# Kernel tuning notes

Hardware: AMD Instinct MI355X
Metric: run time of the kernel (lower is better)

The kernel has to match this reference:

```python
import jax, jax.numpy as jnp
import numpy as np

B, N, HID, NH, NREL, E = 4, 1024, 768, 12, 64, 65536
DH = HID // NH  # 64
TOKEN_TYPE = 0  # NodeType.TOKEN.value


def setup_inputs() -> dict:
    key = jax.random.key(0)
    ks = jax.random.split(key, 24)
    s = 0.02
    inp = {}
    inp["node_states"] = jax.random.normal(ks[0], (B, N, HID), jnp.float32)
    eb = jax.random.randint(ks[1], (E,), 0, B)
    eh = jax.random.randint(ks[2], (E,), 0, N)
    et = jax.random.randint(ks[3], (E,), 0, N)
    er = jax.random.randint(ks[4], (E,), 0, NREL)
    inp["edge_indices"] = jnp.stack([eb, eh, et, er]).astype(jnp.int32)
    inp["node_type_ids"] = jax.random.randint(ks[5], (B, N), 0, 3).astype(jnp.int32)
    names = ["Wq", "Wk", "Wv", "Wq_kb", "Wk_kb", "Wv_kb"]
    for i, nm in enumerate(names):
        inp[nm] = jax.random.normal(ks[6 + i], (HID, HID), jnp.float32) * s
        inp["b" + nm[1:]] = jax.random.normal(ks[12 + i], (HID,), jnp.float32) * s
    inp["rel_mats"] = jax.random.normal(ks[18], (NREL, DH, DH), jnp.float32) * s
    edge_emb = jax.random.normal(ks[19], (NREL, HID), jnp.float32) * s
    inp["edge_emb"] = edge_emb.at[0].set(0.0)  # TOKEN_TO_TOKEN_RELATION_ID row zeroed
    return inp


def reference(node_states, edge_indices, node_type_ids,
              Wq, bq, Wk, bk, Wv, bv,
              Wq_kb, bq_kb, Wk_kb, bk_kb, Wv_kb, bv_kb,
              rel_mats, edge_emb):
    eb, eh, et, er = edge_indices  # (E,) each
    tok = (node_type_ids == TOKEN_TYPE)[..., None]  # (B, N, 1)

    def dual(W_tok, b_tok, W_kb, b_kb):
        # mask_a * tok_proj(x) + mask_b * kb_proj(x)
        return jnp.where(tok, node_states @ W_tok.T + b_tok,
                         node_states @ W_kb.T + b_kb)

    Q = dual(Wq, bq, Wq_kb, bq_kb)  # (B, N, HID)
    K = dual(Wk, bk, Wk_kb, bk_kb)
    V = dual(Wv, bv, Wv_kb, bv_kb)

    # --- attention logits on edges ---
    Qe = Q[eb, eh].reshape(E, NH, DH)  # query at head node
    Ke = K[eb, et].reshape(E, NH, DH)  # key at tail node
    Me = rel_mats[er]                  # (E, DH, DH) per-edge relation matrix
    # (Q @ M) . K per head, scaled
    logits = jnp.einsum('ehd,edf,ehf->eh', Qe, Me, Ke) / jnp.sqrt(
        jnp.asarray(DH, node_states.dtype))  # (E, NH)

    # --- sparse softmax over tail nodes, per (batch, head_node, att_head) ---
    seg = eb * N + eh  # (E,)
    mx = jax.ops.segment_max(logits, seg, num_segments=B * N)  # (B*N, NH)
    ex = jnp.exp(logits - mx[seg])
    denom = jax.ops.segment_sum(ex, seg, num_segments=B * N)
    probs = ex / denom[seg]  # (E, NH); dropout p=0.0 (eval)

    # --- values: V at tail node + edge value embedding ---
    Ve = (V[eb, et] + edge_emb[er]).reshape(E, NH, DH)

    # --- weighted scatter-sum over tail dim ---
    msg = probs[..., None] * Ve  # (E, NH, DH)
    out = jax.ops.segment_sum(msg, seg, num_segments=B * N)  # (B*N, NH, DH)
    return out.reshape(B, N, HID)
```

## Files before the change

### kernel.cpp

```cpp
#include <hip/hip_runtime.h>
#include <math.h>
#include <stdint.h>

#define BB   4
#define NN   1024
#define HID  768
#define NH   12
#define DH   64
#define NREL 64
#define EE   65536
#define NSEG (BB*NN)
#define NOUT 4608
#define UNIT_E 64
#define MAXU (EE/UNIT_E + NREL)
#define NBLK 256
#define MAXMT 34

typedef __bf16 bf16;
typedef __bf16 bf16x8 __attribute__((ext_vector_type(8)));
typedef float  f32x4  __attribute__((ext_vector_type(4)));

__device__ __forceinline__ void load_lds16(const void* g, void* l) {
  __builtin_amdgcn_global_load_lds(
      (__attribute__((address_space(1))) void*)(uintptr_t)g,
      (__attribute__((address_space(3))) void*)(uintptr_t)l, 16, 0, 0);
}

__device__ __forceinline__ int swz(int byte_off) {
  return byte_off ^ (((byte_off >> 7) & 7) << 4);
}

__device__ __forceinline__ float b2f(unsigned short u) {
  return __uint_as_float(((unsigned)u) << 16);
}

__global__ __launch_bounds__(1024)
void partition_kernel(const int* __restrict__ nt, int* __restrict__ origrow,
                      int* __restrict__ meta, int* __restrict__ cnt){
  __shared__ int sums[1024];
  __shared__ int ntot;
  const int t = threadIdx.x;
  int tk[4]; int c = 0;
  #pragma unroll
  for (int i=0;i<4;i++){ tk[i] = (nt[t*4+i]==0); c += tk[i]; cnt[t*4+i] = 0; }
  sums[t]=c; __syncthreads();
  for (int off=1; off<1024; off<<=1){
    const int v = (t>=off) ? sums[t-off] : 0;
    __syncthreads();
    sums[t]+=v;
    __syncthreads();
  }
  if (t==1023) ntot = sums[1023];
  __syncthreads();
  const int excl = sums[t]-c;
  int tokpos = excl, kbpos = ntot + (4*t - excl);
  #pragma unroll
  for (int i=0;i<4;i++){
    if (tk[i]) origrow[tokpos++] = t*4+i;
    else       origrow[kbpos++]  = t*4+i;
  }
  if (t==0){
    const int ntok = ntot, nkb = NSEG - ntok;
    const int tt = (ntok+127)>>7, ktt = (nkb+127)>>7;
    meta[0]=ntok; meta[1]=tt+ktt;
    for (int m=0;m<tt+ktt;m++){
      meta[2+m]  = (m<tt) ? m*128 : ntok + (m-tt)*128;
      meta[40+m] = (m<tt) ? 1 : 0;
    }
  }
}

__global__ __launch_bounds__(256)
void prep_kernel(const float* __restrict__ X, const int* __restrict__ origrow,
                 const float* __restrict__ W0, const float* __restrict__ W1,
                 const float* __restrict__ W2, const float* __restrict__ W3,
                 const float* __restrict__ W4, const float* __restrict__ W5,
                 const float* __restrict__ b0, const float* __restrict__ b1,
                 const float* __restrict__ b2, const float* __restrict__ b3,
                 const float* __restrict__ b4, const float* __restrict__ b5,
                 const float* __restrict__ relm, const float* __restrict__ emb,
                 bf16* __restrict__ Xp, bf16* __restrict__ Wb,
                 float* __restrict__ biasAll, bf16* __restrict__ Mt,
                 bf16* __restrict__ Eb){
  const int blk = blockIdx.x, tid = threadIdx.x;
  if (blk < NSEG) {
    if (tid < 192) {
      const int orig = origrow[blk];
      float4 v = *reinterpret_cast<const float4*>(X + (size_t)orig*HID + tid*4);
      bf16 o[4] = {(bf16)v.x,(bf16)v.y,(bf16)v.z,(bf16)v.w};
      *reinterpret_cast<uint64_t*>(Xp + (size_t)blk*HID + tid*4) = *reinterpret_cast<uint64_t*>(o);
    }
  } else if (blk < NSEG + NOUT) {
    const int r = blk - NSEG;
    const int j = r / HID;
    const int o = r - j * HID;
    const float* Wj; const float* bj;
    if      (j==0){Wj=W0;bj=b0;} else if(j==1){Wj=W1;bj=b1;}
    else if (j==2){Wj=W2;bj=b2;} else if(j==3){Wj=W3;bj=b3;}
    else if (j==4){Wj=W4;bj=b4;} else            {Wj=W5;bj=b5;}
    const float* src = Wj + (size_t)o * HID;
    bf16* dst = Wb + (size_t)r * HID;
    for (int c = tid; c < HID; c += 256) dst[c] = (bf16)src[c];
    if (tid == 0) biasAll[r] = bj[o];
  } else if (blk < NSEG + NOUT + NREL) {
    const int r = blk - NSEG - NOUT;
    const float* M = relm + (size_t)r * DH * DH;
    bf16* o = Mt + (size_t)r * DH * DH;
    for (int i = tid; i < DH * DH; i += 256) {
      const int d = i >> 6, f = i & 63;
      o[f * DH + d] = (bf16)M[i];
    }
  } else {
    const int r = blk - NSEG - NOUT - NREL;
    const float* src = emb + (size_t)r * HID;
    bf16* dst = Eb + (size_t)r * HID;
    for (int c = tid; c < HID; c += 256) dst[c] = (bf16)src[c];
  }
}

#define BM 128
#define BN 128
#define BK 32
#define NT (HID/BK)
#define NCT 18
#define NWG (MAXMT*NCT)

__global__ __launch_bounds__(256)
void gemm_kernel(const bf16* __restrict__ A, const bf16* __restrict__ Bw,
                 const float* __restrict__ biasAll, const int* __restrict__ origrow,
                 const int* __restrict__ meta,
                 bf16* __restrict__ Qb, bf16* __restrict__ Kb, bf16* __restrict__ Vb)
{
  __shared__ bf16 As[3][BM * BK];
  __shared__ bf16 Bs[3][BN * BK];

  const int orig = blockIdx.x;
  const int xcd  = orig & 7;
  const int wg   = (xcd < 4 ? xcd * 77 : 4 * 77 + (xcd - 4) * 76) + (orig >> 3);
  const int mt   = wg / NCT;
  const int ctt  = wg - mt * NCT;

  const int ntok = meta[0], nmt = meta[1];
  if (mt >= nmt) return;
  const int base  = meta[2+mt];
  const int istok = meta[40+mt];

  const int tid  = threadIdx.x;
  const int lane = tid & 63;
  const int w    = tid >> 6;
  const int wrow = w >> 1, wcol = w & 1;
  const int ct_local = ctt * BN;
  const int brow0 = (istok ? 0 : 2304) + ct_local;

  f32x4 acc[4][4];
  #pragma unroll
  for (int mi=0;mi<4;mi++)
    #pragma unroll
    for (int ni=0;ni<4;ni++) acc[mi][ni] = (f32x4){0.f,0.f,0.f,0.f};

  const char* Ab = (const char*)A;
  const char* Bb = (const char*)Bw;

  int rowg[2], inrowg[2], Pg[2];
  #pragma unroll
  for (int i = 0; i < 2; ++i) {
    const int P = (i * 256 + tid) * 16;
    const int L = swz(P);
    Pg[i] = P; rowg[i] = L >> 6; inrowg[i] = L & 63;
  }

  #define STAGE(kt, b)                                                              \
    { _Pragma("unroll")                                                             \
      for (int i = 0; i < 2; ++i) {                                                 \
        load_lds16(Ab + ((size_t)(base  + rowg[i]) * HID + (kt) * BK) * 2 + inrowg[i], \
                   (char*)As[b] + Pg[i]);                                           \
        load_lds16(Bb + ((size_t)(brow0 + rowg[i]) * HID + (kt) * BK) * 2 + inrowg[i], \
                   (char*)Bs[b] + Pg[i]);                                           \
      } }

  STAGE(0, 0);
  STAGE(1, 1);

  for (int kt = 0; kt < NT; ++kt) {
    if (kt < NT - 1) asm volatile("s_waitcnt vmcnt(4)" ::: "memory");
    else             asm volatile("s_waitcnt vmcnt(0)" ::: "memory");
    __builtin_amdgcn_s_barrier();
    if (kt + 2 < NT) { STAGE(kt + 2, (kt + 2) % 3); }

    const char* Asb = (const char*)As[kt % 3];
    const char* Bsb = (const char*)Bs[kt % 3];
    bf16x8 af[4], bfr[4];
    #pragma unroll
    for (int mi = 0; mi < 4; ++mi) {
      const int r = wrow * 64 + mi * 16 + (lane & 15);
      const int L = r * 64 + (lane >> 4) * 16;
      af[mi] = *reinterpret_cast<const bf16x8*>(Asb + swz(L));
    }
    #pragma unroll
    for (int ni = 0; ni < 4; ++ni) {
      const int r = wcol * 64 + ni * 16 + (lane & 15);
      const int L = r * 64 + (lane >> 4) * 16;
      bfr[ni] = *reinterpret_cast<const bf16x8*>(Bsb + swz(L));
    }
    #pragma unroll
    for (int mi = 0; mi < 4; ++mi)
      #pragma unroll
      for (int ni = 0; ni < 4; ++ni)
        acc[mi][ni] = __builtin_amdgcn_mfma_f32_16x16x32_bf16(af[mi], bfr[ni], acc[mi][ni], 0, 0, 0);
  }

  const int j3 = ct_local / HID;
  const int o0 = ct_local - j3 * HID;
  const int rowLim = istok ? ntok : NSEG;
  const int bidx0 = (istok ? j3 : j3 + 3) * HID + o0;
  #pragma unroll
  for (int mi = 0; mi < 4; ++mi) {
    #pragma unroll
    for (int i = 0; i < 4; ++i) {
      const int rr = base + wrow * 64 + mi * 16 + (lane >> 4) * 4 + i;
      if (rr < rowLim) {
        const int orig2 = origrow[rr];
        #pragma unroll
        for (int ni = 0; ni < 4; ++ni) {
          const int cg = wcol * 64 + ni * 16 + (lane & 15);
          const float val = acc[mi][ni][i] + biasAll[bidx0 + cg];
          if (j3 == 2)      Vb[(size_t)orig2 * HID + o0 + cg] = (bf16)val;
          else if (j3 == 0) Qb[(size_t)orig2 * HID + o0 + cg] = (bf16)val;
          else              Kb[(size_t)orig2 * HID + o0 + cg] = (bf16)val;
        }
      }
    }
  }
}

__global__ __launch_bounds__(256)
void hist_both_kernel(const int* __restrict__ ei, int* __restrict__ cnt,
                      int* __restrict__ cnt_blk){
  __shared__ int lc[NREL];
  const int tid = threadIdx.x, blk = blockIdx.x;
  if (tid < NREL) lc[tid] = 0;
  __syncthreads();
  const int e = blk*256 + tid;
  atomicAdd(&cnt[ei[e]*NN + ei[EE+e]], 1);
  atomicAdd(&lc[ei[3*EE+e]], 1);
  __syncthreads();
  if (tid < NREL) cnt_blk[tid*NBLK + blk] = lc[tid];
}

__global__ __launch_bounds__(1024)
void scan_both_kernel(const int* __restrict__ cnt, int* __restrict__ start,
                      int* __restrict__ cursor, int* __restrict__ cnt_blk,
                      int* __restrict__ start_rel, int* __restrict__ cnt_rel,
                      int* __restrict__ ustart){
  __shared__ int sums[1024];
  const int t = threadIdx.x;
  if (blockIdx.x == 0) {
    const int c0=cnt[t*4], c1=cnt[t*4+1], c2=cnt[t*4+2], c3=cnt[t*4+3];
    const int s = c0+c1+c2+c3;
    sums[t]=s; __syncthreads();
    for (int off=1; off<1024; off<<=1){
      const int v = (t>=off) ? sums[t-off] : 0;
      __syncthreads();
      sums[t]+=v;
      __syncthreads();
    }
    const int excl = sums[t]-s;
    const int o0=excl, o1=o0+c0, o2=o1+c1, o3=o2+c2;
    start[t*4]=o0;  start[t*4+1]=o1;  start[t*4+2]=o2;  start[t*4+3]=o3;
    cursor[t*4]=o0; cursor[t*4+1]=o1; cursor[t*4+2]=o2; cursor[t*4+3]=o3;
  } else {
    int v[16]; int s = 0;
    #pragma unroll
    for (int i=0;i<16;i++){ v[i] = cnt_blk[t*16+i]; s += v[i]; }
    sums[t] = s; __syncthreads();
    for (int off=1; off<1024; off<<=1){
      const int x = (t>=off) ? sums[t-off] : 0;
      __syncthreads();
      sums[t] += x;
      __syncthreads();
    }
    int run = sums[t] - s;
    #pragma unroll
    for (int i=0;i<16;i++){ const int c = v[i]; cnt_blk[t*16+i] = run; run += c; }
    __syncthreads();
    if (t < NREL) {
      const int st  = cnt_blk[t*NBLK];
      const int nxt = (t == NREL-1) ? EE : cnt_blk[(t+1)*NBLK];
      const int c   = nxt - st;
      start_rel[t] = st;
      cnt_rel[t]   = c;
      const int units = (c + UNIT_E - 1) / UNIT_E;
      int su = units;
      #pragma unroll
      for (int off=1; off<64; off<<=1) {
        const int vu = __shfl_up(su, off);
        if (t >= off) su += vu;
      }
      ustart[t] = su - units;
      if (t == NREL-1) ustart[NREL] = su;
    }
  }
}

__global__ __launch_bounds__(256)
void scatter_both_kernel(const int* __restrict__ ei, int* __restrict__ cursor,
                         int* __restrict__ order, const int* __restrict__ base_blk,
                         int* __restrict__ order_rel){
  __shared__ int lc[NREL];
  const int tid = threadIdx.x, blk = blockIdx.x;
  if (tid < NREL) lc[tid] = 0;
  __syncthreads();
  const int e = blk*256 + tid;
  const int seg = ei[e]*NN + ei[EE+e];
  order[atomicAdd(&cursor[seg], 1)] = e;
  const int r = ei[3*EE + e];
  const int rank = atomicAdd(&lc[r], 1);
  order_rel[base_blk[r*NBLK + blk] + rank] = e;
}

__global__ __launch_bounds__(256)
void logits_mfma_kernel(const bf16* __restrict__ Qb, const bf16* __restrict__ Kb,
                        const int* __restrict__ ei, const bf16* __restrict__ Mt,
                        const int* __restrict__ order_rel, const int* __restrict__ start_rel,
                        const int* __restrict__ cnt_rel, const int* __restrict__ ustart,
                        float* __restrict__ L)
{
  __shared__ int qoff[UNIT_E], koff[UNIT_E], eidx[UNIT_E];
  __shared__ int us[NREL+1];
  __shared__ int relsh;
  const int tid = threadIdx.x;
  const int u = blockIdx.x;
  if (tid < NREL+1) us[tid] = ustart[tid];
  __syncthreads();
  if (u >= us[NREL]) return;
  if (tid < NREL && us[tid] <= u && u < us[tid+1]) relsh = tid;
  __syncthreads();
  const int r = relsh;
  const int lu = u - us[r];
  const int ebase = start_rel[r] + lu * UNIT_E;
  const int nvalid = min(UNIT_E, cnt_rel[r] - lu * UNIT_E);
  if (tid < UNIT_E) {
    const int epos = ebase + (tid < nvalid ? tid : 0);
    const int e = order_rel[epos];
    eidx[tid] = (tid < nvalid) ? e : -1;
    const int eb = ei[e], eh = ei[EE+e], et = ei[2*EE+e];
    qoff[tid] = (eb*NN + eh) * HID;
    koff[tid] = (eb*NN + et) * HID;
  }
  __syncthreads();

  const int w = tid >> 6, lane = tid & 63;
  const int l15 = lane & 15, lg = lane >> 4;
  const bf16* Mr = Mt + (size_t)r * DH * DH;
  bf16x8 bfr[4][2];
  #pragma unroll
  for (int ni = 0; ni < 4; ++ni)
    #pragma unroll
    for (int kk = 0; kk < 2; ++kk)
      bfr[ni][kk] = *reinterpret_cast<const bf16x8*>(
          Mr + (ni*16 + l15) * DH + kk*32 + lg*8);

  #define LOADQ(mt, a0, a1)                                              \
    { const int lr = (mt)*16 + l15;                                      \
      const int el = lr / 12, hh = lr - el*12;                           \
      const int qo = qoff[w*16 + el] + hh*64 + lg*8;                     \
      a0 = *reinterpret_cast<const bf16x8*>(Qb + qo);                    \
      a1 = *reinterpret_cast<const bf16x8*>(Qb + qo + 32); }

  #define LOADK(mt, kr)                                                  \
    { _Pragma("unroll")                                                  \
      for (int i = 0; i < 4; ++i) {                                      \
        const int lr2 = (mt)*16 + lg*4 + i;                              \
        const int el2 = lr2 / 12, h2 = lr2 - el2*12;                     \
        const int ko = koff[w*16 + el2] + h2*64 + l15;                   \
        _Pragma("unroll")                                                \
        for (int ni = 0; ni < 4; ++ni)                                   \
          kr[i*4+ni] = *reinterpret_cast<const unsigned short*>(Kb + ko + ni*16); } }

  #define COMPUTE(mt, a0, a1, kr)                                        \
    { f32x4 acc_[4];                                                     \
      _Pragma("unroll")                                                  \
      for (int ni = 0; ni < 4; ++ni) {                                   \
        acc_[ni] = (f32x4){0.f,0.f,0.f,0.f};                             \
        acc_[ni] = __builtin_amdgcn_mfma_f32_16x16x32_bf16(a0, bfr[ni][0], acc_[ni], 0, 0, 0); \
        acc_[ni] = __builtin_amdgcn_mfma_f32_16x16x32_bf16(a1, bfr[ni][1], acc_[ni], 0, 0, 0); \
      }                                                                  \
      _Pragma("unroll")                                                  \
      for (int i = 0; i < 4; ++i) {                                      \
        const int lr2 = (mt)*16 + lg*4 + i;                              \
        const int el2 = lr2 / 12, h2 = lr2 - el2*12;                     \
        float p = acc_[0][i]*b2f(kr[i*4+0]) + acc_[1][i]*b2f(kr[i*4+1])  \
                + acc_[2][i]*b2f(kr[i*4+2]) + acc_[3][i]*b2f(kr[i*4+3]); \
        p += __shfl_xor(p, 1); p += __shfl_xor(p, 2);                    \
        p += __shfl_xor(p, 4); p += __shfl_xor(p, 8);                    \
        if (l15 == 0) {                                                  \
          const int e = eidx[w*16 + el2];                                \
          if (e >= 0) L[(size_t)e*NH + h2] = p * 0.125f;                 \
        } } }

  bf16x8 a0A, a1A, a0B, a1B;
  unsigned short krA[16], krB[16];
  LOADQ(0, a0A, a1A); LOADK(0, krA);
  #pragma unroll
  for (int mt = 0; mt < 12; mt += 2) {
    LOADQ(mt+1, a0B, a1B); LOADK(mt+1, krB);
    COMPUTE(mt, a0A, a1A, krA);
    if (mt + 2 < 12) { LOADQ(mt+2, a0A, a1A); LOADK(mt+2, krA); }
    COMPUTE(mt+1, a0B, a1B, krB);
  }
  #undef LOADQ
  #undef LOADK
  #undef COMPUTE
}

#define SEGCAP 128
__global__ __launch_bounds__(256)
void segout_kernel(const int* __restrict__ ei, const bf16* __restrict__ Vb,
                   const bf16* __restrict__ Eb, const float* __restrict__ L,
                   const int* __restrict__ start, const int* __restrict__ cnt,
                   const int* __restrict__ order, float* __restrict__ out)
{
  const int s = blockIdx.x, tid = threadIdx.x;
  float* o = out + (size_t)s*HID;
  const int n = cnt[s];
  if (n==0){ o[tid]=0.f; o[tid+256]=0.f; o[tid+512]=0.f; return; }

  __shared__ float denom[NH];
  __shared__ float inv[NH];
  const int st = start[s];
  const int eb = s >> 10;
  const int h0 = tid >> 6;

  if (tid<NH) denom[tid]=0.f;

  if (n <= SEGCAP) {
    __shared__ float pr[SEGCAP*NH];
    __shared__ int voffs[SEGCAP];
    __shared__ int eoffs[SEGCAP];
    if (tid < n) {
      const int e = order[st + tid];
      voffs[tid] = (eb*NN + ei[2*EE+e]) * HID;
      eoffs[tid] = ei[3*EE+e] * HID;
    }
    __syncthreads();
    for (int idx=tid; idx<n*NH; idx+=256){
      const int e = order[st + idx/NH];
      const float v = expf(L[(size_t)e*NH + idx - (idx/NH)*NH]);
      pr[idx] = v;
      atomicAdd(&denom[idx - (idx/NH)*NH], v);
    }
    __syncthreads();
    if (tid<NH) inv[tid] = 1.f/denom[tid];
    __syncthreads();
    const float i0=inv[h0], i1=inv[h0+4], i2=inv[h0+8];
    float a0=0.f, a1=0.f, a2=0.f;
    float b0_=0.f, b1_=0.f, b2_=0.f;
    int i = 0;
    for (; i+1<n; i+=2){
      const bf16* vrA = Vb + voffs[i];
      const bf16* erA = Eb + eoffs[i];
      const bf16* vrB = Vb + voffs[i+1];
      const bf16* erB = Eb + eoffs[i+1];
      const float pA0 = pr[i*NH+h0  ]*i0, pB0 = pr[(i+1)*NH+h0  ]*i0;
      const float pA1 = pr[i*NH+h0+4]*i1, pB1 = pr[(i+1)*NH+h0+4]*i1;
      const float pA2 = pr[i*NH+h0+8]*i2, pB2 = pr[(i+1)*NH+h0+8]*i2;
      a0  += pA0*(b2f(*(const unsigned short*)(vrA+tid    ))+b2f(*(const unsigned short*)(erA+tid    )));
      b0_ += pB0*(b2f(*(const unsigned short*)(vrB+tid    ))+b2f(*(const unsigned short*)(erB+tid    )));
      a1  += pA1*(b2f(*(const unsigned short*)(vrA+tid+256))+b2f(*(const unsigned short*)(erA+tid+256)));
      b1_ += pB1*(b2f(*(const unsigned short*)(vrB+tid+256))+b2f(*(const unsigned short*)(erB+tid+256)));
      a2  += pA2*(b2f(*(const unsigned short*)(vrA+tid+512))+b2f(*(const unsigned short*)(erA+tid+512)));
      b2_ += pB2*(b2f(*(const unsigned short*)(vrB+tid+512))+b2f(*(const unsigned short*)(erB+tid+512)));
    }
    if (i < n) {
      const bf16* vr = Vb + voffs[i];
      const bf16* erow = Eb + eoffs[i];
      const float p0 = pr[i*NH+h0  ]*i0;
      const float p1 = pr[i*NH+h0+4]*i1;
      const float p2 = pr[i*NH+h0+8]*i2;
      a0 += p0*(b2f(*(const unsigned short*)(vr+tid    ))+b2f(*(const unsigned short*)(erow+tid    )));
      a1 += p1*(b2f(*(const unsigned short*)(vr+tid+256))+b2f(*(const unsigned short*)(erow+tid+256)));
      a2 += p2*(b2f(*(const unsigned short*)(vr+tid+512))+b2f(*(const unsigned short*)(erow+tid+512)));
    }
    o[tid]=a0+b0_; o[tid+256]=a1+b1_; o[tid+512]=a2+b2_;
  } else {
    __syncthreads();
    for (int i=tid; i<n*NH; i+=256){
      const int e = order[st + i/NH];
      atomicAdd(&denom[i - (i/NH)*NH], expf(L[(size_t)e*NH + i - (i/NH)*NH]));
    }
    __syncthreads();
    if (tid<NH) inv[tid] = 1.f/denom[tid];
    __syncthreads();
    const float i0=inv[h0], i1=inv[h0+4], i2=inv[h0+8];
    float a0=0.f, a1=0.f, a2=0.f;
    for (int i=0;i<n;i++){
      const int e  = order[st+i];
      const int et = ei[2*EE+e], er = ei[3*EE+e];
      const bf16* vr = Vb + (size_t)(eb*NN+et)*HID;
      const bf16* erow = Eb + (size_t)er*HID;
      const float p0 = expf(L[(size_t)e*NH+h0  ])*i0;
      const float p1 = expf(L[(size_t)e*NH+h0+4])*i1;
      const float p2 = expf(L[(size_t)e*NH+h0+8])*i2;
      a0 += p0*(b2f(*(const unsigned short*)(vr+tid    ))+b2f(*(const unsigned short*)(erow+tid    )));
      a1 += p1*(b2f(*(const unsigned short*)(vr+tid+256))+b2f(*(const unsigned short*)(erow+tid+256)));
      a2 += p2*(b2f(*(const unsigned short*)(vr+tid+512))+b2f(*(const unsigned short*)(erow+tid+512)));
    }
    o[tid]=a0; o[tid+256]=a1; o[tid+512]=a2;
  }
}

extern "C" void kernel_launch(void* const* d_in, const int* in_sizes, int n_in,
                              void* d_out, int out_size, void* d_ws, size_t ws_size,
                              hipStream_t stream)
{
  const float* X  = (const float*)d_in[0];
  const int*   ei = (const int*)d_in[1];
  const int*   nt = (const int*)d_in[2];
  const float* W[6]; const float* bia[6];
  for (int j=0;j<6;j++){ W[j]=(const float*)d_in[3+2*j]; bia[j]=(const float*)d_in[4+2*j]; }
  const float* relm = (const float*)d_in[15];
  const float* emb  = (const float*)d_in[16];
  float* out = (float*)d_out;

  char* p = (char*)d_ws;
  bf16*  Qb = (bf16*)p;  p += (size_t)NSEG*HID*2;
  bf16*  Kb = (bf16*)p;  p += (size_t)NSEG*HID*2;
  bf16*  Vb = (bf16*)p;  p += (size_t)NSEG*HID*2;
  float* L  = (float*)p; p += (size_t)EE*NH*4;
  int* cnt      = (int*)p; p += NSEG*4;
  int* start    = (int*)p; p += NSEG*4;
  int* cursor   = (int*)p; p += NSEG*4;
  int* order    = (int*)p; p += (size_t)EE*4;
  int* cnt_blk    = (int*)p; p += NREL*NBLK*4;
  int* start_rel  = (int*)p; p += NREL*4;
  int* cnt_rel    = (int*)p; p += NREL*4;
  int* ustart     = (int*)p; p += (NREL+4)*4;
  int* order_rel  = (int*)p; p += (size_t)EE*4;
  int* origrow    = (int*)p; p += (NSEG+128)*4;
  int* meta       = (int*)p; p += 80*4;
  bf16* Xp = (bf16*)p;  p += (size_t)(NSEG+128)*HID*2;
  bf16* Wb = (bf16*)p;  p += (size_t)NOUT*HID*2;
  bf16* Mt = (bf16*)p;  p += (size_t)NREL*DH*DH*2;
  bf16* Eb = (bf16*)p;  p += (size_t)NREL*HID*2;
  float* biasAll = (float*)p; p += NOUT*4;

  partition_kernel<<<1, 1024, 0, stream>>>(nt, origrow, meta, cnt);
  prep_kernel<<<NSEG + NOUT + NREL + NREL, 256, 0, stream>>>(X, origrow,
      W[0],W[1],W[2],W[3],W[4],W[5],
      bia[0],bia[1],bia[2],bia[3],bia[4],bia[5], relm, emb, Xp, Wb, biasAll, Mt, Eb);
  gemm_kernel<<<NWG, 256, 0, stream>>>(Xp, Wb, biasAll, origrow,
      meta, Qb, Kb, Vb);

  hist_both_kernel<<<NBLK, 256, 0, stream>>>(ei, cnt, cnt_blk);
  scan_both_kernel<<<2, 1024, 0, stream>>>(cnt, start, cursor, cnt_blk,
      start_rel, cnt_rel, ustart);
  scatter_both_kernel<<<NBLK, 256, 0, stream>>>(ei, cursor, order, cnt_blk, order_rel);

  logits_mfma_kernel<<<MAXU, 256, 0, stream>>>(Qb, Kb, ei, Mt, order_rel,
      start_rel, cnt_rel, ustart, L);
  segout_kernel<<<NSEG, 256, 0, stream>>>(ei, Vb, Eb, L, start, cnt, order, out);
}
```

Before: 141.4 us.

## Fuse histogram into prep kernel and compute softmax denominators in logits kernel

```diff
diff --git a/kernel.cpp b/kernel.cpp
--- a/kernel.cpp
+++ b/kernel.cpp
@@ -36,13 +36,15 @@
 
 __global__ __launch_bounds__(1024)
 void partition_kernel(const int* __restrict__ nt, int* __restrict__ origrow,
-                      int* __restrict__ meta, int* __restrict__ cnt){
+                      int* __restrict__ meta, int* __restrict__ cnt,
+                      float* __restrict__ denomG){
   __shared__ int sums[1024];
   __shared__ int ntot;
   const int t = threadIdx.x;
   int tk[4]; int c = 0;
   #pragma unroll
   for (int i=0;i<4;i++){ tk[i] = (nt[t*4+i]==0); c += tk[i]; cnt[t*4+i] = 0; }
+  for (int i=t; i<NSEG*NH; i+=1024) denomG[i] = 0.f;
   sums[t]=c; __syncthreads();
   for (int off=1; off<1024; off<<=1){
     const int v = (t>=off) ? sums[t-off] : 0;
@@ -79,9 +81,12 @@
                  const float* __restrict__ b2, const float* __restrict__ b3,
                  const float* __restrict__ b4, const float* __restrict__ b5,
                  const float* __restrict__ relm, const float* __restrict__ emb,
+                 const int* __restrict__ ei,
                  bf16* __restrict__ Xp, bf16* __restrict__ Wb,
                  float* __restrict__ biasAll, bf16* __restrict__ Mt,
-                 bf16* __restrict__ Eb){
+                 bf16* __restrict__ Eb, int* __restrict__ cnt,
+                 int* __restrict__ cnt_blk){
+  __shared__ int lc[NREL];
   const int blk = blockIdx.x, tid = threadIdx.x;
   if (blk < NSEG) {
     if (tid < 192) {
@@ -110,11 +115,20 @@
       const int d = i >> 6, f = i & 63;
       o[f * DH + d] = (bf16)M[i];
     }
-  } else {
+  } else if (blk < NSEG + NOUT + 2*NREL) {
     const int r = blk - NSEG - NOUT - NREL;
     const float* src = emb + (size_t)r * HID;
     bf16* dst = Eb + (size_t)r * HID;
     for (int c = tid; c < HID; c += 256) dst[c] = (bf16)src[c];
+  } else {
+    const int blk2 = blk - (NSEG + NOUT + 2*NREL);
+    if (tid < NREL) lc[tid] = 0;
+    __syncthreads();
+    const int e = blk2*256 + tid;
+    atomicAdd(&cnt[ei[e]*NN + ei[EE+e]], 1);
+    atomicAdd(&lc[ei[3*EE+e]], 1);
+    __syncthreads();
+    if (tid < NREL) cnt_blk[tid*NBLK + blk2] = lc[tid];
   }
 }
 
@@ -231,20 +245,6 @@
       }
     }
   }
-}
-
-__global__ __launch_bounds__(256)
-void hist_both_kernel(const int* __restrict__ ei, int* __restrict__ cnt,
-                      int* __restrict__ cnt_blk){
-  __shared__ int lc[NREL];
-  const int tid = threadIdx.x, blk = blockIdx.x;
-  if (tid < NREL) lc[tid] = 0;
-  __syncthreads();
-  const int e = blk*256 + tid;
-  atomicAdd(&cnt[ei[e]*NN + ei[EE+e]], 1);
-  atomicAdd(&lc[ei[3*EE+e]], 1);
-  __syncthreads();
-  if (tid < NREL) cnt_blk[tid*NBLK + blk] = lc[tid];
 }
 
 __global__ __launch_bounds__(1024)
@@ -323,9 +323,9 @@
                         const int* __restrict__ ei, const bf16* __restrict__ Mt,
                         const int* __restrict__ order_rel, const int* __restrict__ start_rel,
                         const int* __restrict__ cnt_rel, const int* __restrict__ ustart,
-                        float* __restrict__ L)
+                        float* __restrict__ L, float* __restrict__ dG)
 {
-  __shared__ int qoff[UNIT_E], koff[UNIT_E], eidx[UNIT_E];
+  __shared__ int qoff[UNIT_E], koff[UNIT_E], eidx[UNIT_E], sgb[UNIT_E];
   __shared__ int us[NREL+1];
   __shared__ int relsh;
   const int tid = threadIdx.x;
@@ -346,6 +346,7 @@
     const int eb = ei[e], eh = ei[EE+e], et = ei[2*EE+e];
     qoff[tid] = (eb*NN + eh) * HID;
     koff[tid] = (eb*NN + et) * HID;
+    sgb[tid]  = (eb*NN + eh) * NH;
   }
   __syncthreads();
 
@@ -395,7 +396,11 @@
         p += __shfl_xor(p, 4); p += __shfl_xor(p, 8);                    \
         if (l15 == 0) {                                                  \
           const int e = eidx[w*16 + el2];                                \
-          if (e >= 0) L[(size_t)e*NH + h2] = p * 0.125f;                 \
+          if (e >= 0) {                                                  \
+            const float ex = __expf(p * 0.125f);                         \
+            L[(size_t)e*NH + h2] = ex;                                   \
+            atomicAdd(&dG[sgb[w*16 + el2] + h2], ex);                    \
+          }                                                              \
         } } }
 
   bf16x8 a0A, a1A, a0B, a1B;
@@ -418,39 +423,34 @@
 void segout_kernel(const int* __restrict__ ei, const bf16* __restrict__ Vb,
                    const bf16* __restrict__ Eb, const float* __restrict__ L,
                    const int* __restrict__ start, const int* __restrict__ cnt,
-                   const int* __restrict__ order, float* __restrict__ out)
+                   const int* __restrict__ order, const float* __restrict__ denomG,
+                   float* __restrict__ out)
 {
   const int s = blockIdx.x, tid = threadIdx.x;
   float* o = out + (size_t)s*HID;
   const int n = cnt[s];
   if (n==0){ o[tid]=0.f; o[tid+256]=0.f; o[tid+512]=0.f; return; }
 
-  __shared__ float denom[NH];
   __shared__ float inv[NH];
+  __shared__ float pr[SEGCAP*NH];
+  __shared__ int voffs[SEGCAP];
+  __shared__ int eoffs[SEGCAP];
   const int st = start[s];
   const int eb = s >> 10;
   const int h0 = tid >> 6;
 
-  if (tid<NH) denom[tid]=0.f;
+  if (tid<NH) inv[tid] = 1.f/denomG[s*NH + tid];
 
   if (n <= SEGCAP) {
-    __shared__ float pr[SEGCAP*NH];
-    __shared__ int voffs[SEGCAP];
-    __shared__ int eoffs[SEGCAP];
     if (tid < n) {
       const int e = order[st + tid];
       voffs[tid] = (eb*NN + ei[2*EE+e]) * HID;
       eoffs[tid] = ei[3*EE+e] * HID;
     }
-    __syncthreads();
     for (int idx=tid; idx<n*NH; idx+=256){
       const int e = order[st + idx/NH];
-      const float v = expf(L[(size_t)e*NH + idx - (idx/NH)*NH]);
-      pr[idx] = v;
-      atomicAdd(&denom[idx - (idx/NH)*NH], v);
-    }
-    __syncthreads();
-    if (tid<NH) inv[tid] = 1.f/denom[tid];
+      pr[idx] = L[(size_t)e*NH + idx - (idx/NH)*NH];
+    }
     __syncthreads();
     const float i0=inv[h0], i1=inv[h0+4], i2=inv[h0+8];
     float a0=0.f, a1=0.f, a2=0.f;
@@ -484,13 +484,6 @@
     o[tid]=a0+b0_; o[tid+256]=a1+b1_; o[tid+512]=a2+b2_;
   } else {
     __syncthreads();
-    for (int i=tid; i<n*NH; i+=256){
-      const int e = order[st + i/NH];
-      atomicAdd(&denom[i - (i/NH)*NH], expf(L[(size_t)e*NH + i - (i/NH)*NH]));
-    }
-    __syncthreads();
-    if (tid<NH) inv[tid] = 1.f/denom[tid];
-    __syncthreads();
     const float i0=inv[h0], i1=inv[h0+4], i2=inv[h0+8];
     float a0=0.f, a1=0.f, a2=0.f;
     for (int i=0;i<n;i++){
@@ -498,9 +491,9 @@
       const int et = ei[2*EE+e], er = ei[3*EE+e];
       const bf16* vr = Vb + (size_t)(eb*NN+et)*HID;
       const bf16* erow = Eb + (size_t)er*HID;
-      const float p0 = expf(L[(size_t)e*NH+h0  ])*i0;
-      const float p1 = expf(L[(size_t)e*NH+h0+4])*i1;
-      const float p2 = expf(L[(size_t)e*NH+h0+8])*i2;
+      const float p0 = L[(size_t)e*NH+h0  ]*i0;
+      const float p1 = L[(size_t)e*NH+h0+4]*i1;
+      const float p2 = L[(size_t)e*NH+h0+8]*i2;
       a0 += p0*(b2f(*(const unsigned short*)(vr+tid    ))+b2f(*(const unsigned short*)(erow+tid    )));
       a1 += p1*(b2f(*(const unsigned short*)(vr+tid+256))+b2f(*(const unsigned short*)(erow+tid+256)));
       a2 += p2*(b2f(*(const unsigned short*)(vr+tid+512))+b2f(*(const unsigned short*)(erow+tid+512)));
@@ -538,25 +531,26 @@
   int* order_rel  = (int*)p; p += (size_t)EE*4;
   int* origrow    = (int*)p; p += (NSEG+128)*4;
   int* meta       = (int*)p; p += 80*4;
+  float* denomG   = (float*)p; p += (size_t)NSEG*NH*4;
   bf16* Xp = (bf16*)p;  p += (size_t)(NSEG+128)*HID*2;
   bf16* Wb = (bf16*)p;  p += (size_t)NOUT*HID*2;
   bf16* Mt = (bf16*)p;  p += (size_t)NREL*DH*DH*2;
   bf16* Eb = (bf16*)p;  p += (size_t)NREL*HID*2;
   float* biasAll = (float*)p; p += NOUT*4;
 
-  partition_kernel<<<1, 1024, 0, stream>>>(nt, origrow, meta, cnt);
-  prep_kernel<<<NSEG + NOUT + NREL + NREL, 256, 0, stream>>>(X, origrow,
+  partition_kernel<<<1, 1024, 0, stream>>>(nt, origrow, meta, cnt, denomG);
+  prep_kernel<<<NSEG + NOUT + 2*NREL + NBLK, 256, 0, stream>>>(X, origrow,
       W[0],W[1],W[2],W[3],W[4],W[5],
-      bia[0],bia[1],bia[2],bia[3],bia[4],bia[5], relm, emb, Xp, Wb, biasAll, Mt, Eb);
+      bia[0],bia[1],bia[2],bia[3],bia[4],bia[5], relm, emb, ei,
+      Xp, Wb, biasAll, Mt, Eb, cnt, cnt_blk);
   gemm_kernel<<<NWG, 256, 0, stream>>>(Xp, Wb, biasAll, origrow,
       meta, Qb, Kb, Vb);
 
-  hist_both_kernel<<<NBLK, 256, 0, stream>>>(ei, cnt, cnt_blk);
   scan_both_kernel<<<2, 1024, 0, stream>>>(cnt, start, cursor, cnt_blk,
       start_rel, cnt_rel, ustart);
   scatter_both_kernel<<<NBLK, 256, 0, stream>>>(ei, cursor, order, cnt_blk, order_rel);
 
   logits_mfma_kernel<<<MAXU, 256, 0, stream>>>(Qb, Kb, ei, Mt, order_rel,
-      start_rel, cnt_rel, ustart, L);
-  segout_kernel<<<NSEG, 256, 0, stream>>>(ei, Vb, Eb, L, start, cnt, order, out);
-}
+      start_rel, cnt_rel, ustart, L, denomG);
+  segout_kernel<<<NSEG, 256, 0, stream>>>(ei, Vb, Eb, L, start, cnt, order, denomG, out);
+}
```

Result: slower. 149.3 us (+5.5%).
